# Optimization experiments

Measured on AMD Instinct MI355X. Metric: run time of the kernel, lower is better.

## Reference

```python
import jax, jax.numpy as jnp
import numpy as np

HEADS = 8
DIM_HEAD = 64
SCALE = DIM_HEAD ** -0.5
K = 7


def _conv(x, w, stride):
    return jax.lax.conv_general_dilated(
        x, w, window_strides=(stride, stride), padding='VALID',
        dimension_numbers=('NHWC', 'HWIO', 'NHWC'))


def _split_heads(t):
    # 'b x y (h d) -> (b h) (x y) d'
    b, X, Y, hd = t.shape
    d = hd // HEADS
    t = t.reshape(b, X, Y, HEADS, d)
    t = t.transpose(0, 3, 1, 2, 4)  # b h x y d
    return t.reshape(b * HEADS, X * Y, d)


def setup_inputs() -> dict:
    key = jax.random.key(0)
    ks = jax.random.split(key, 6)
    dim, inner = 256, HEADS * DIM_HEAD
    x = jax.random.normal(ks[0], (8, 84, 84, dim), dtype=jnp.float32)
    w_q = jax.random.normal(ks[1], (1, 1, dim, inner), dtype=jnp.float32) * 0.02
    w_kv = jax.random.normal(ks[2], (K, K, dim, 2 * inner), dtype=jnp.float32) * 0.02
    w_out = jax.random.normal(ks[3], (1, 1, inner, dim), dtype=jnp.float32) * 0.02
    b_out = jnp.zeros((dim,), dtype=jnp.float32)
    return {"x": x, "w_q": w_q, "w_kv": w_kv, "w_out": w_out, "b_out": b_out}


def reference(x, w_q, w_kv, w_out, b_out):
    b, X, Y, _ = x.shape
    q = _conv(x, w_q, 1)          # [b, X, Y, inner]
    kv = _conv(x, w_kv, K)        # [b, X/k, Y/k, 2*inner]
    k, v = jnp.split(kv, 2, axis=-1)
    q = _split_heads(q)           # [(b h), XY, d]
    k = _split_heads(k)           # [(b h), xy, d]
    v = _split_heads(v)
    dots = jnp.einsum('bid,bjd->bij', q, k) * SCALE
    attn = jax.nn.softmax(dots, axis=-1)
    out = jnp.einsum('bij,bjd->bid', attn, v)  # [(b h), XY, d]
    out = out.reshape(b, HEADS, X, Y, DIM_HEAD).transpose(0, 2, 3, 1, 4)
    out = out.reshape(b, X, Y, HEADS * DIM_HEAD)
    out = _conv(out, w_out, 1) + b_out  # dropout rate 0 -> identity
    return out
```

## Files before the change

kernel.cpp:

```cpp
#include <hip/hip_runtime.h>

typedef unsigned short u16;
typedef __bf16 bf16x8 __attribute__((ext_vector_type(8)));
typedef __bf16 bf16x4 __attribute__((ext_vector_type(4)));
typedef float f32x4 __attribute__((ext_vector_type(4)));

__device__ __forceinline__ u16 f2b(float f) {
    __bf16 h = (__bf16)f;
    return __builtin_bit_cast(u16, h);
}
__device__ __forceinline__ unsigned pk2(float a, float b) {
    return (unsigned)f2b(a) | ((unsigned)f2b(b) << 16);
}

__device__ __forceinline__ int xcd_chunk(int wg, int n) {
    int q = n >> 3, r = n & 7;
    int x = wg & 7, i = wg >> 3;
    return (x < r ? x * (q + 1) : r * (q + 1) + (x - r) * q) + i;
}

#define GLOAD_LDS16(src, dst)                                              \
    __builtin_amdgcn_global_load_lds(                                      \
        (const __attribute__((address_space(1))) void*)(src),              \
        (__attribute__((address_space(3))) void*)(dst), 16, 0, 0)

__global__ __launch_bounds__(256) void k_pack_x(const float* __restrict__ x,
                                                u16* __restrict__ xp) {
    int v = blockIdx.x * 256 + threadIdx.x;
    int c0 = (v & 31) << 3;
    int pix = v >> 5;
    int b = pix / 7056;
    int r = pix - b * 7056;
    int y = r / 84;
    int xx = r - y * 84;
    int opix = (b * 144 + (y / 7) * 12 + (xx / 7)) * 49 + (y % 7) * 7 + (xx % 7);
    const float4* src = reinterpret_cast<const float4*>(x + ((size_t)pix << 8) + c0);
    float4 f0 = src[0], f1 = src[1];
    bf16x8 o = {(__bf16)f0.x, (__bf16)f0.y, (__bf16)f0.z, (__bf16)f0.w,
                (__bf16)f1.x, (__bf16)f1.y, (__bf16)f1.z, (__bf16)f1.w};
    *reinterpret_cast<bf16x8*>(xp + ((size_t)opix << 8) + c0) = o;
}

__global__ __launch_bounds__(256) void k_tconv(const float* __restrict__ in,
                                               u16* __restrict__ out, int R, int C,
                                               float scale, int permk) {
    __shared__ float tile[32][33];
    int c0 = blockIdx.x << 5, r0 = blockIdx.y << 5;
    int tx = threadIdx.x, ty = threadIdx.y;
#pragma unroll
    for (int i = 0; i < 4; i++)
        tile[ty + (i << 3)][tx] = in[(size_t)(r0 + ty + (i << 3)) * C + c0 + tx];
    __syncthreads();
    int k = r0 + tx;
    int kw = permk ? ((k & ~63) | ((k & 15) << 2) | ((k >> 4) & 3)) : k;
#pragma unroll
    for (int i = 0; i < 4; i++)
        out[(size_t)(c0 + ty + (i << 3)) * R + kw] = f2b(tile[tx][ty + (i << 3)] * scale);
}

__global__ __launch_bounds__(256) void k_kvproj(const u16* __restrict__ xp,
                                                const u16* __restrict__ wkvT,
                                                float* __restrict__ parts) {
    __shared__ u16 As[8192];
    __shared__ u16 Bs[4096];
    const int lin = xcd_chunk(blockIdx.x, 576);
    const int mt = lin % 9;
    const int rest = lin / 9;
    const int nt = rest & 15;
    const int sp = rest >> 4;
    const int tid = threadIdx.x;
    const int wave = tid >> 6, lane = tid & 63;
    const int wr = wave >> 1, wc = wave & 1;
    const int lrow = lane & 15, lkg = lane >> 4;
    const u16* Ag = xp + (size_t)(mt * 128) * 12544 + sp * 3136;
    const u16* Bg = wkvT + (size_t)(nt * 64) * 12544 + sp * 3136;
    const int srow = lane >> 3;
    const int scol_sw = (((lane & 7) ^ srow) << 3);
    f32x4 acc[4][2];
#pragma unroll
    for (int m = 0; m < 4; m++)
#pragma unroll
        for (int n = 0; n < 2; n++)
#pragma unroll
            for (int i = 0; i < 4; i++) acc[m][n][i] = 0.f;

    for (int ks = 0; ks < 49; ks++) {
        const int k0 = ks << 6;
        __syncthreads();
#pragma unroll
        for (int j = 0; j < 4; j++) {
            const int c = (wave << 2) + j;
            const int row = (c << 3) + srow;
            GLOAD_LDS16(Ag + (size_t)row * 12544 + k0 + scol_sw, As + (c << 9));
        }
#pragma unroll
        for (int j = 0; j < 2; j++) {
            const int c = (wave << 1) + j;
            const int row = (c << 3) + srow;
            GLOAD_LDS16(Bg + (size_t)row * 12544 + k0 + scol_sw, Bs + (c << 9));
        }
        __syncthreads();
#pragma unroll
        for (int kk = 0; kk < 2; kk++) {
            const int sig = (kk << 2) + lkg;
            const int sw = ((sig ^ (lrow & 7)) << 3);
            bf16x8 a[4], bb[2];
#pragma unroll
            for (int m = 0; m < 4; m++)
                a[m] = *reinterpret_cast<const bf16x8*>(As + (((wr << 6) + (m << 4) + lrow) << 6) + sw);
#pragma unroll
            for (int n = 0; n < 2; n++)
                bb[n] = *reinterpret_cast<const bf16x8*>(Bs + (((wc << 5) + (n << 4) + lrow) << 6) + sw);
#pragma unroll
            for (int m = 0; m < 4; m++)
#pragma unroll
                for (int n = 0; n < 2; n++)
                    acc[m][n] = __builtin_amdgcn_mfma_f32_16x16x32_bf16(a[m], bb[n], acc[m][n], 0, 0, 0);
        }
    }
    float* outp = parts + (size_t)sp * 1179648;
#pragma unroll
    for (int m = 0; m < 4; m++)
#pragma unroll
        for (int n = 0; n < 2; n++)
#pragma unroll
            for (int i = 0; i < 4; i++) {
                int row = (mt << 7) + (wr << 6) + (m << 4) + (lkg << 2) + i;
                int col = (nt << 6) + (wc << 5) + (n << 4) + lrow;
                outp[(size_t)row * 1024 + col] = acc[m][n][i];
            }
}

__global__ __launch_bounds__(256) void k_kvfin(const float* __restrict__ parts,
                                               u16* __restrict__ Kf, u16* __restrict__ Vf) {
    int v = blockIdx.x * 256 + threadIdx.x;
    int m = v >> 8;
    int n0 = (v & 255) << 2;
    float4 s = {0.f, 0.f, 0.f, 0.f};
#pragma unroll
    for (int sp = 0; sp < 4; sp++) {
        float4 p = *reinterpret_cast<const float4*>(parts + (size_t)sp * 1179648 +
                                                    (size_t)m * 1024 + n0);
        s.x += p.x; s.y += p.y; s.z += p.z; s.w += p.w;
    }
    int b = m / 144, pi = m - b * 144;
    float sv[4] = {s.x, s.y, s.z, s.w};
#pragma unroll
    for (int e4 = 0; e4 < 4; e4++) {
        int n = n0 + e4;
        int h = (n & 511) >> 6, d = n & 63;
        int bh = (b << 3) + h;
        if (n < 512) {
            int fc = pi >> 4, lr = pi & 15;
            int ks = d >> 5, lg = (d >> 3) & 3, e = d & 7;
            Kf[((((size_t)bh * 9 + fc) << 1) + ks) * 512 + (((lg << 4) + lr) << 3) + e] = f2b(sv[e4]);
        } else {
            int nf = d >> 4, lr = d & 15;
            int ks = pi >> 5;
            int e = (((pi >> 4) & 1) << 2) | (pi & 3);
            int lg = (pi >> 2) & 3;
            Vf[(((size_t)bh * 4 + nf) * 5 + ks) * 512 + (((lg << 4) + lr) << 3) + e] = f2b(sv[e4]);
        }
    }
}

__global__ __launch_bounds__(256) void k_qproj(const u16* __restrict__ xp,
                                               const u16* __restrict__ wqT,
                                               u16* __restrict__ Qf) {
    __shared__ u16 As[128][72];
    __shared__ u16 Bs[128][72];
    const int lin = xcd_chunk(blockIdx.x, 1764);
    const int nt = lin & 3, mt = lin >> 2;
    const int tid = threadIdx.x;
    const int wave = tid >> 6, lane = tid & 63;
    const int wr = wave >> 1, wc = wave & 1;
    const int lrow = lane & 15, lkg = lane >> 4;
    const u16* Ag = xp + (size_t)(mt * 128) * 256;
    const u16* Bg = wqT + (size_t)(nt * 128) * 256;
    const int srow = tid >> 3, scol = (tid & 7) << 3;
    f32x4 acc[4][4];
#pragma unroll
    for (int m = 0; m < 4; m++)
#pragma unroll
        for (int n = 0; n < 4; n++)
#pragma unroll
            for (int i = 0; i < 4; i++) acc[m][n][i] = 0.f;

    for (int ks = 0; ks < 4; ks++) {
        const int k0 = ks * 64;
        __syncthreads();
#pragma unroll
        for (int p = 0; p < 4; p++) {
            int rr = srow + (p << 5);
            *reinterpret_cast<bf16x8*>(&As[rr][scol]) =
                *reinterpret_cast<const bf16x8*>(Ag + (size_t)rr * 256 + k0 + scol);
            *reinterpret_cast<bf16x8*>(&Bs[rr][scol]) =
                *reinterpret_cast<const bf16x8*>(Bg + (size_t)rr * 256 + k0 + scol);
        }
        __syncthreads();
#pragma unroll
        for (int kk = 0; kk < 2; kk++) {
            const int ko = (kk << 5) + (lkg << 3);
            bf16x8 a[4], bb[4];
#pragma unroll
            for (int m = 0; m < 4; m++)
                a[m] = *reinterpret_cast<const bf16x8*>(&As[(wr << 6) + (m << 4) + lrow][ko]);
#pragma unroll
            for (int n = 0; n < 4; n++)
                bb[n] = *reinterpret_cast<const bf16x8*>(&Bs[(wc << 6) + (n << 4) + lrow][ko]);
#pragma unroll
            for (int m = 0; m < 4; m++)
#pragma unroll
                for (int n = 0; n < 4; n++)
                    acc[m][n] = __builtin_amdgcn_mfma_f32_16x16x32_bf16(a[m], bb[n], acc[m][n], 0, 0, 0);
        }
    }
#pragma unroll
    for (int m = 0; m < 4; m++)
#pragma unroll
        for (int n = 0; n < 4; n++)
#pragma unroll
            for (int i = 0; i < 4; i++) {
                int row = (mt << 7) + (wr << 6) + (m << 4) + (lkg << 2) + i;
                int col = (nt << 7) + (wc << 6) + (n << 4) + lrow;
                int b = row / 7056, pp = row - b * 7056;
                int h = col >> 6, d = col & 63;
                int bh = (b << 3) + h;
                int tt = pp >> 4, flr = pp & 15;
                int fks = d >> 5, flg = (d >> 3) & 3, fe = d & 7;
                Qf[((((size_t)bh * 441 + tt) << 1) + fks) * 512 + (((flg << 4) + flr) << 3) + fe] =
                    f2b(acc[m][n][i]);
            }
}

__global__ __launch_bounds__(128, 4) void k_attn(const u16* __restrict__ Qf,
                                                 const u16* __restrict__ Kf,
                                                 const u16* __restrict__ Vf,
                                                 u16* __restrict__ O) {
    const int wv = threadIdx.x >> 6, lane = threadIdx.x & 63;
    const int t = blockIdx.x;
    const int h = (blockIdx.y << 1) + wv;
    const int b = blockIdx.z;
    const int lrow = lane & 15, lkg = lane >> 4;
    const int bh = (b << 3) + h;
    const int l8 = lane << 3;

    const u16* Qg = Qf + ((((size_t)bh * 441 + t) << 1) << 9);
    const u16* Kg = Kf + (((size_t)bh * 9) << 10);
    const u16* Vg = Vf + ((size_t)bh * 20) * 512;

    f32x4 da[9];
#pragma unroll
    for (int fc = 0; fc < 9; fc++)
#pragma unroll
        for (int i = 0; i < 4; i++) da[fc][i] = 0.f;
#pragma unroll
    for (int ks = 0; ks < 2; ks++) {
        bf16x8 aq = *reinterpret_cast<const bf16x8*>(Qg + (ks << 9) + l8);
#pragma unroll
        for (int fc = 0; fc < 9; fc++) {
            bf16x8 bk = *reinterpret_cast<const bf16x8*>(Kg + ((((fc << 1) + ks)) << 9) + l8);
            da[fc] = __builtin_amdgcn_mfma_f32_16x16x32_bf16(bk, aq, da[fc], 0, 0, 0);
        }
    }

    float mx = -1e30f;
#pragma unroll
    for (int fc = 0; fc < 9; fc++)
#pragma unroll
        for (int i = 0; i < 4; i++) mx = fmaxf(mx, da[fc][i]);
    mx = fmaxf(mx, __shfl_xor(mx, 16));
    mx = fmaxf(mx, __shfl_xor(mx, 32));
    float sum = 0.f;
#pragma unroll
    for (int fc = 0; fc < 9; fc++)
#pragma unroll
        for (int i = 0; i < 4; i++) {
            float v = __expf(da[fc][i] - mx);
            da[fc][i] = v;
            sum += v;
        }
    sum += __shfl_xor(sum, 16);
    sum += __shfl_xor(sum, 32);
    float inv = 1.0f / sum;
    unsigned pw[9][2];
#pragma unroll
    for (int fc = 0; fc < 9; fc++) {
        pw[fc][0] = pk2(da[fc][0] * inv, da[fc][1] * inv);
        pw[fc][1] = pk2(da[fc][2] * inv, da[fc][3] * inv);
    }

    f32x4 oa[4];
#pragma unroll
    for (int n = 0; n < 4; n++)
#pragma unroll
        for (int i = 0; i < 4; i++) oa[n][i] = 0.f;
#pragma unroll
    for (int ks = 0; ks < 5; ks++) {
        uint4 pav;
        if (ks < 4)
            pav = uint4{pw[2 * ks][0], pw[2 * ks][1], pw[2 * ks + 1][0], pw[2 * ks + 1][1]};
        else
            pav = uint4{pw[8][0], pw[8][1], 0u, 0u};
        bf16x8 pa = __builtin_bit_cast(bf16x8, pav);
#pragma unroll
        for (int n = 0; n < 4; n++) {
            bf16x8 bv = *reinterpret_cast<const bf16x8*>(Vg + ((size_t)(n * 5 + ks) << 9) + l8);
            oa[n] = __builtin_amdgcn_mfma_f32_16x16x32_bf16(pa, bv, oa[n], 0, 0, 0);
        }
    }

#pragma unroll
    for (int i = 0; i < 4; i++) {
        int r = (lkg << 2) + i;
        int q = (t << 4) + r;
        int pi = q / 49, pos = q - pi * 49;
        int y = (pi / 12) * 7 + pos / 7;
        int xx = (pi - (pi / 12) * 12) * 7 + (pos - (pos / 7) * 7);
        bf16x4 ov = {(__bf16)oa[0][i], (__bf16)oa[1][i], (__bf16)oa[2][i], (__bf16)oa[3][i]};
        *reinterpret_cast<bf16x4*>(O + (((size_t)b * 7056 + y * 84 + xx) << 9) +
                                   (h << 6) + (lrow << 2)) = ov;
    }
}

__global__ __launch_bounds__(256) void k_outproj(const u16* __restrict__ A,
                                                 const u16* __restrict__ BT,
                                                 const float* __restrict__ bias,
                                                 float* __restrict__ out) {
    __shared__ u16 As[128][72];
    __shared__ u16 Bs[128][72];
    const int lin = xcd_chunk(blockIdx.x, 882);
    const int nt = lin & 1, mt = lin >> 1;
    const int tid = threadIdx.x;
    const int wave = tid >> 6, lane = tid & 63;
    const int wr = wave >> 1, wc = wave & 1;
    const int lrow = lane & 15, lkg = lane >> 4;
    const u16* Ag = A + (size_t)(mt * 128) * 512;
    const u16* Bg = BT + (size_t)(nt * 128) * 512;
    const int srow = tid >> 3, scol = (tid & 7) << 3;
    f32x4 acc[4][4];
#pragma unroll
    for (int m = 0; m < 4; m++)
#pragma unroll
        for (int n = 0; n < 4; n++)
#pragma unroll
            for (int i = 0; i < 4; i++) acc[m][n][i] = 0.f;

    for (int ks = 0; ks < 8; ks++) {
        const int k0 = ks * 64;
        __syncthreads();
#pragma unroll
        for (int p = 0; p < 4; p++) {
            int rr = srow + (p << 5);
            *reinterpret_cast<bf16x8*>(&As[rr][scol]) =
                *reinterpret_cast<const bf16x8*>(Ag + (size_t)rr * 512 + k0 + scol);
            *reinterpret_cast<bf16x8*>(&Bs[rr][scol]) =
                *reinterpret_cast<const bf16x8*>(Bg + (size_t)rr * 512 + k0 + scol);
        }
        __syncthreads();
#pragma unroll
        for (int kk = 0; kk < 2; kk++) {
            const int ko = (kk << 5) + (lkg << 3);
            bf16x8 a[4], bb[4];
#pragma unroll
            for (int m = 0; m < 4; m++)
                a[m] = *reinterpret_cast<const bf16x8*>(&As[(wr << 6) + (m << 4) + lrow][ko]);
#pragma unroll
            for (int n = 0; n < 4; n++)
                bb[n] = *reinterpret_cast<const bf16x8*>(&Bs[(wc << 6) + (n << 4) + lrow][ko]);
#pragma unroll
            for (int m = 0; m < 4; m++)
#pragma unroll
                for (int n = 0; n < 4; n++)
                    acc[m][n] = __builtin_amdgcn_mfma_f32_16x16x32_bf16(a[m], bb[n], acc[m][n], 0, 0, 0);
        }
    }
#pragma unroll
    for (int m = 0; m < 4; m++)
#pragma unroll
        for (int n = 0; n < 4; n++)
#pragma unroll
            for (int i = 0; i < 4; i++) {
                int row = (mt << 7) + (wr << 6) + (m << 4) + (lkg << 2) + i;
                int col = (nt << 7) + (wc << 6) + (n << 4) + lrow;
                out[(size_t)row * 256 + col] = acc[m][n][i] + bias[col];
            }
}

extern "C" void kernel_launch(void* const* d_in, const int* in_sizes, int n_in,
                              void* d_out, int out_size, void* d_ws, size_t ws_size,
                              hipStream_t stream) {
    const float* x = (const float*)d_in[0];
    const float* w_q = (const float*)d_in[1];
    const float* w_kv = (const float*)d_in[2];
    const float* w_out = (const float*)d_in[3];
    const float* b_out = (const float*)d_in[4];
    float* out = (float*)d_out;

    char* ws = (char*)d_ws;
    size_t off = 0;
    auto alloc = [&](size_t bytes) -> char* {
        char* p = ws + off;
        off = (off + bytes + 255) & ~(size_t)255;
        return p;
    };
    u16* xp = (u16*)alloc(28901376ull);
    u16* wqT = (u16*)alloc(262144ull);
    u16* woutT = (u16*)alloc(262144ull);
    u16* Kf = (u16*)alloc(1179648ull);
    u16* Vf = (u16*)alloc(1310720ull);
    u16* O = (u16*)alloc(57802752ull);
    u16* wkvT = (u16*)alloc(25690112ull);
    float* parts = (float*)alloc(33030144ull);
    u16* Qf = (u16*)wkvT;

    hipMemsetAsync(Vf, 0, 1310720ull, stream);
    k_pack_x<<<7056, 256, 0, stream>>>(x, xp);
    k_tconv<<<dim3(32, 392), dim3(32, 8), 0, stream>>>(w_kv, wkvT, 12544, 1024, 1.0f, 0);
    k_tconv<<<dim3(16, 8), dim3(32, 8), 0, stream>>>(w_q, wqT, 256, 512, 0.125f, 0);
    k_tconv<<<dim3(8, 16), dim3(32, 8), 0, stream>>>(w_out, woutT, 512, 256, 1.0f, 1);
    k_kvproj<<<576, 256, 0, stream>>>(xp, wkvT, parts);
    k_kvfin<<<1152, 256, 0, stream>>>(parts, Kf, Vf);
    k_qproj<<<1764, 256, 0, stream>>>(xp, wqT, Qf);
    k_attn<<<dim3(441, 4, 8), 128, 0, stream>>>(Qf, Kf, Vf, O);
    k_outproj<<<882, 256, 0, stream>>>(O, woutT, b_out, out);
}
```

Baseline: 224.6 us.

## Keep K/V fragments in registers across three query tiles per attention block

Each attention workgroup now loads its head's K and V fragments into registers once and loops over three query tiles, so K/V reloads and the number of launched blocks both drop by a factor of three. The output scatter address math (divisions by 49, 12, 7) is replaced by a small precomputed lookup table built by a new kernel. In exchange the kernel holds many more live registers, the occupancy hint drops from 4 to 2 blocks per SIMD, and there is one extra tiny launch.

After: 221.3 us. About the same (-1.5%).

```diff
diff --git a/kernel.cpp b/kernel.cpp
--- a/kernel.cpp
+++ b/kernel.cpp
@@ -39,6 +39,15 @@
     bf16x8 o = {(__bf16)f0.x, (__bf16)f0.y, (__bf16)f0.z, (__bf16)f0.w,
                 (__bf16)f1.x, (__bf16)f1.y, (__bf16)f1.z, (__bf16)f1.w};
     *reinterpret_cast<bf16x8*>(xp + ((size_t)opix << 8) + c0) = o;
+}
+
+__global__ __launch_bounds__(256) void k_lut(int* __restrict__ lut) {
+    int q = blockIdx.x * 256 + threadIdx.x;
+    if (q >= 7056) return;
+    int pi = q / 49, pos = q - pi * 49;
+    int y = (pi / 12) * 7 + pos / 7;
+    int xx = (pi - (pi / 12) * 12) * 7 + (pos - (pos / 7) * 7);
+    lut[q] = y * 84 + xx;
 }
 
 __global__ __launch_bounds__(256) void k_tconv(const float* __restrict__ in,
@@ -233,93 +242,104 @@
             }
 }
 
-__global__ __launch_bounds__(128, 4) void k_attn(const u16* __restrict__ Qf,
+__global__ __launch_bounds__(128, 2) void k_attn(const u16* __restrict__ Qf,
                                                  const u16* __restrict__ Kf,
                                                  const u16* __restrict__ Vf,
+                                                 const int* __restrict__ lut,
                                                  u16* __restrict__ O) {
     const int wv = threadIdx.x >> 6, lane = threadIdx.x & 63;
-    const int t = blockIdx.x;
     const int h = (blockIdx.y << 1) + wv;
     const int b = blockIdx.z;
     const int lrow = lane & 15, lkg = lane >> 4;
     const int bh = (b << 3) + h;
     const int l8 = lane << 3;
 
-    const u16* Qg = Qf + ((((size_t)bh * 441 + t) << 1) << 9);
     const u16* Kg = Kf + (((size_t)bh * 9) << 10);
     const u16* Vg = Vf + ((size_t)bh * 20) * 512;
 
-    f32x4 da[9];
+    bf16x8 kf[9][2], vf[4][5];
 #pragma unroll
     for (int fc = 0; fc < 9; fc++)
 #pragma unroll
-        for (int i = 0; i < 4; i++) da[fc][i] = 0.f;
-#pragma unroll
-    for (int ks = 0; ks < 2; ks++) {
-        bf16x8 aq = *reinterpret_cast<const bf16x8*>(Qg + (ks << 9) + l8);
+        for (int ks = 0; ks < 2; ks++)
+            kf[fc][ks] = *reinterpret_cast<const bf16x8*>(Kg + (((fc << 1) + ks) << 9) + l8);
+#pragma unroll
+    for (int n = 0; n < 4; n++)
+#pragma unroll
+        for (int ks = 0; ks < 5; ks++)
+            vf[n][ks] = *reinterpret_cast<const bf16x8*>(Vg + ((size_t)(n * 5 + ks) << 9) + l8);
+
+    const int t0 = blockIdx.x * 3;
+#pragma unroll 1
+    for (int jt = 0; jt < 3; jt++) {
+        const int t = t0 + jt;
+        const u16* Qg = Qf + ((((size_t)bh * 441 + t) << 1) << 9);
+
+        f32x4 da[9];
+#pragma unroll
+        for (int fc = 0; fc < 9; fc++)
+#pragma unroll
+            for (int i = 0; i < 4; i++) da[fc][i] = 0.f;
+#pragma unroll
+        for (int ks = 0; ks < 2; ks++) {
+            bf16x8 aq = *reinterpret_cast<const bf16x8*>(Qg + (ks << 9) + l8);
+#pragma unroll
+            for (int fc = 0; fc < 9; fc++)
+                da[fc] = __builtin_amdgcn_mfma_f32_16x16x32_bf16(kf[fc][ks], aq, da[fc], 0, 0, 0);
+        }
+
+        float mx = -1e30f;
+#pragma unroll
+        for (int fc = 0; fc < 9; fc++)
+#pragma unroll
+            for (int i = 0; i < 4; i++) mx = fmaxf(mx, da[fc][i]);
+        mx = fmaxf(mx, __shfl_xor(mx, 16));
+        mx = fmaxf(mx, __shfl_xor(mx, 32));
+        float sum = 0.f;
+#pragma unroll
+        for (int fc = 0; fc < 9; fc++)
+#pragma unroll
+            for (int i = 0; i < 4; i++) {
+                float v = __expf(da[fc][i] - mx);
+                da[fc][i] = v;
+                sum += v;
+            }
+        sum += __shfl_xor(sum, 16);
+        sum += __shfl_xor(sum, 32);
+        float inv = 1.0f / sum;
+        unsigned pw[9][2];
 #pragma unroll
         for (int fc = 0; fc < 9; fc++) {
-            bf16x8 bk = *reinterpret_cast<const bf16x8*>(Kg + ((((fc << 1) + ks)) << 9) + l8);
-            da[fc] = __builtin_amdgcn_mfma_f32_16x16x32_bf16(bk, aq, da[fc], 0, 0, 0);
-        }
-    }
-
-    float mx = -1e30f;
-#pragma unroll
-    for (int fc = 0; fc < 9; fc++)
-#pragma unroll
-        for (int i = 0; i < 4; i++) mx = fmaxf(mx, da[fc][i]);
-    mx = fmaxf(mx, __shfl_xor(mx, 16));
-    mx = fmaxf(mx, __shfl_xor(mx, 32));
-    float sum = 0.f;
-#pragma unroll
-    for (int fc = 0; fc < 9; fc++)
+            pw[fc][0] = pk2(da[fc][0] * inv, da[fc][1] * inv);
+            pw[fc][1] = pk2(da[fc][2] * inv, da[fc][3] * inv);
+        }
+
+        f32x4 oa[4];
+#pragma unroll
+        for (int n = 0; n < 4; n++)
+#pragma unroll
+            for (int i = 0; i < 4; i++) oa[n][i] = 0.f;
+#pragma unroll
+        for (int ks = 0; ks < 5; ks++) {
+            uint4 pav;
+            if (ks < 4)
+                pav = uint4{pw[2 * ks][0], pw[2 * ks][1], pw[2 * ks + 1][0], pw[2 * ks + 1][1]};
+            else
+                pav = uint4{pw[8][0], pw[8][1], 0u, 0u};
+            bf16x8 pa = __builtin_bit_cast(bf16x8, pav);
+#pragma unroll
+            for (int n = 0; n < 4; n++)
+                oa[n] = __builtin_amdgcn_mfma_f32_16x16x32_bf16(pa, vf[n][ks], oa[n], 0, 0, 0);
+        }
+
 #pragma unroll
         for (int i = 0; i < 4; i++) {
-            float v = __expf(da[fc][i] - mx);
-            da[fc][i] = v;
-            sum += v;
-        }
-    sum += __shfl_xor(sum, 16);
-    sum += __shfl_xor(sum, 32);
-    float inv = 1.0f / sum;
-    unsigned pw[9][2];
-#pragma unroll
-    for (int fc = 0; fc < 9; fc++) {
-        pw[fc][0] = pk2(da[fc][0] * inv, da[fc][1] * inv);
-        pw[fc][1] = pk2(da[fc][2] * inv, da[fc][3] * inv);
-    }
-
-    f32x4 oa[4];
-#pragma unroll
-    for (int n = 0; n < 4; n++)
-#pragma unroll
-        for (int i = 0; i < 4; i++) oa[n][i] = 0.f;
-#pragma unroll
-    for (int ks = 0; ks < 5; ks++) {
-        uint4 pav;
-        if (ks < 4)
-            pav = uint4{pw[2 * ks][0], pw[2 * ks][1], pw[2 * ks + 1][0], pw[2 * ks + 1][1]};
-        else
-            pav = uint4{pw[8][0], pw[8][1], 0u, 0u};
-        bf16x8 pa = __builtin_bit_cast(bf16x8, pav);
-#pragma unroll
-        for (int n = 0; n < 4; n++) {
-            bf16x8 bv = *reinterpret_cast<const bf16x8*>(Vg + ((size_t)(n * 5 + ks) << 9) + l8);
-            oa[n] = __builtin_amdgcn_mfma_f32_16x16x32_bf16(pa, bv, oa[n], 0, 0, 0);
-        }
-    }
-
-#pragma unroll
-    for (int i = 0; i < 4; i++) {
-        int r = (lkg << 2) + i;
-        int q = (t << 4) + r;
-        int pi = q / 49, pos = q - pi * 49;
-        int y = (pi / 12) * 7 + pos / 7;
-        int xx = (pi - (pi / 12) * 12) * 7 + (pos - (pos / 7) * 7);
-        bf16x4 ov = {(__bf16)oa[0][i], (__bf16)oa[1][i], (__bf16)oa[2][i], (__bf16)oa[3][i]};
-        *reinterpret_cast<bf16x4*>(O + (((size_t)b * 7056 + y * 84 + xx) << 9) +
-                                   (h << 6) + (lrow << 2)) = ov;
+            int q = (t << 4) + (lkg << 2) + i;
+            int rast = lut[q];
+            bf16x4 ov = {(__bf16)oa[0][i], (__bf16)oa[1][i], (__bf16)oa[2][i], (__bf16)oa[3][i]};
+            *reinterpret_cast<bf16x4*>(O + (((size_t)b * 7056 + rast) << 9) +
+                                       (h << 6) + (lrow << 2)) = ov;
+        }
     }
 }
 
@@ -409,12 +429,14 @@
     u16* woutT = (u16*)alloc(262144ull);
     u16* Kf = (u16*)alloc(1179648ull);
     u16* Vf = (u16*)alloc(1310720ull);
+    int* lut = (int*)alloc(28416ull);
     u16* O = (u16*)alloc(57802752ull);
     u16* wkvT = (u16*)alloc(25690112ull);
     float* parts = (float*)alloc(33030144ull);
     u16* Qf = (u16*)wkvT;
 
     hipMemsetAsync(Vf, 0, 1310720ull, stream);
+    k_lut<<<28, 256, 0, stream>>>(lut);
     k_pack_x<<<7056, 256, 0, stream>>>(x, xp);
     k_tconv<<<dim3(32, 392), dim3(32, 8), 0, stream>>>(w_kv, wkvT, 12544, 1024, 1.0f, 0);
     k_tconv<<<dim3(16, 8), dim3(32, 8), 0, stream>>>(w_q, wqT, 256, 512, 0.125f, 0);
@@ -422,6 +444,6 @@
     k_kvproj<<<576, 256, 0, stream>>>(xp, wkvT, parts);
     k_kvfin<<<1152, 256, 0, stream>>>(parts, Kf, Vf);
     k_qproj<<<1764, 256, 0, stream>>>(xp, wqT, Qf);
-    k_attn<<<dim3(441, 4, 8), 128, 0, stream>>>(Qf, Kf, Vf, O);
+    k_attn<<<dim3(147, 4, 8), 128, 0, stream>>>(Qf, Kf, Vf, lut, O);
     k_outproj<<<882, 256, 0, stream>>>(O, woutT, b_out, out);
 }
```
